# Kernel tuning notes

Hardware: AMD Instinct MI355X
Metric: run time of the kernel (lower is better)

## Reference

```python
import jax, jax.numpy as jnp
import numpy as np

H = 16          # bit depth
N_K = 2         # random masks per flipped bit
TP = 8          # location dims per node
CUR_TP = 4      # dims updated per step
CUR_PORTION = 0.8
N = 1 << H      # location value range
T = 1024        # stations
S = 64          # neighbors per station
D = 256         # embedding dim
C = 2 * H * N_K + 1  # candidate locations per station


def _cos_sim(a, b):
    # frexp-based integer 'cosine' similarity from CritiGraph.cos_similarity
    sg = jnp.where(a >= 0, 1.0, -1.0) * jnp.where(b >= 0, 1.0, -1.0)
    x = ((jnp.abs(a) ^ jnp.abs(b)) + 1).astype(jnp.float32)
    _, e = jnp.frexp(x)  # exponent = bit length of (xor+1)
    return sg * (1.0 - e.astype(jnp.float32) / H)


def _connection(ori, rand_numbers):
    # ori: [T,tp] int64, rand_numbers: [T,H,N_K,tp] int64 in [0, N)
    bits = jnp.int64(1) << jnp.arange(H, dtype=jnp.int64)          # [H]
    flipped = ori[:, None, :] ^ bits[None, :, None]                # [T,H,tp]
    masks = rand_numbers & (bits - 1)[None, :, None, None]        # low-k-bit masks
    res = (flipped[:, :, None, :] ^ masks).reshape(ori.shape[0], H * N_K, TP)
    # candidate order: flipped variants, original (index H*N_K ... wait: res has H*N_K), original, negated
    return jnp.concatenate([res, ori[:, None, :], -res], axis=1)  # [T,C,tp]


def setup_inputs() -> dict:
    key = jax.random.key(0)
    ks = jax.random.split(key, 8)
    return {
        "sta_loc": jax.random.randint(ks[0], (T, TP), 1 - N, N, dtype=jnp.int64),
        "nei_loc": jax.random.randint(ks[1], (T, S, TP), 1 - N, N, dtype=jnp.int64),
        "rand_numbers": jax.random.randint(ks[2], (T, H, N_K, TP), 0, N, dtype=jnp.int64),
        "sta_emb": jax.random.normal(ks[3], (T, D), dtype=jnp.float32),
        "nei_emb": jax.random.normal(ks[4], (T, S, D), dtype=jnp.float32),
        "mask": (jax.random.uniform(ks[5], (T, S)) > 0.1).astype(jnp.float32),
        "rand_vals": jax.random.uniform(ks[6], (T, TP), dtype=jnp.float32),
        "t_rand": jax.random.uniform(ks[7], (T,), dtype=jnp.float32),
    }


def _forward(sta_loc, nei_loc, rand_numbers, sta_emb, nei_emb, mask, rand_vals, t_rand):
    cnc_loc = _connection(sta_loc, rand_numbers)                    # [T,C,tp]
    # euclidean-space cosine targets
    sta_n = sta_emb / jnp.linalg.norm(sta_emb, axis=-1, keepdims=True)
    nei_n = nei_emb / jnp.linalg.norm(nei_emb, axis=-1, keepdims=True)
    eu_val = jnp.einsum("td,tsd->ts", sta_n, nei_n)                 # [T,S]
    # ct_val swap-one-dim kernel (= ct_val_triton math)
    cos_sn = _cos_sim(sta_loc[:, None, :], nei_loc)                 # [T,S,tp]
    cos_sn_sum = cos_sn.sum(axis=-1)                                # [T,S]
    cos_cn = _cos_sim(cnc_loc[:, None, :, :], nei_loc[:, :, None, :])  # [T,S,C,tp]
    ct_val = (cos_sn_sum[:, :, None, None] - cos_sn[:, :, None, :] + cos_cn) / TP
    # masked squared cosine loss (loom_valid)
    lth = mask.sum(axis=1) + 1e-12                                  # [T]
    eu = eu_val[:, :, None, None]
    loss = jnp.square(ct_val - eu) * jnp.abs(eu) * mask[:, :, None, None]
    loss = loss.sum(axis=1) / lth[:, None, None]                    # [T,C,tp]
    # get_best_loc argmin routing
    argmin_all = jnp.argmin(loss, axis=1)                           # [T,tp]
    base = jnp.full((T, TP), H * N_K, dtype=argmin_all.dtype)       # index of original loc
    rand_cols = jnp.argsort(rand_vals, axis=1)[:, :CUR_TP]          # [T,cur_tp]
    sel = t_rand < CUR_PORTION                                      # [T]
    rows = jnp.broadcast_to(jnp.arange(T)[:, None], (T, CUR_TP))
    upd = jnp.where(sel[:, None], argmin_all[rows, rand_cols], base[rows, rand_cols])
    cnc_idx = base.at[rows, rand_cols].set(upd)                     # [T,tp]
    ti = jnp.arange(T)[:, None]
    di = jnp.arange(TP)[None, :]
    selected_locs = cnc_loc[ti, cnc_idx, di]                        # [T,tp]
    real_loss = loss[ti, cnc_idx, di].mean(axis=-1)                 # [T]
    return selected_locs, real_loss


def reference(sta_loc, nei_loc, rand_numbers, sta_emb, nei_emb, mask, rand_vals, t_rand):
    return _forward(sta_loc, nei_loc, rand_numbers, sta_emb, nei_emb, mask, rand_vals, t_rand)
```

## Files before the change

kernel.cpp:

```cpp
#include <hip/hip_runtime.h>
#include <math.h>

#define T_ 1024

__device__ __forceinline__ unsigned icode(int v) {
    return (v < 0) ? (0x80000000u | (unsigned)(-v)) : (unsigned)v;
}

__device__ __forceinline__ float cosc(unsigned ca, unsigned cb) {
    unsigned y = ca ^ cb;
    int x = (int)(y & 0x7fffffffu) + 1;
    float m = fmaf((float)__clz(x), 0.0625f, -1.0f);
    return __uint_as_float(__float_as_uint(m) ^ (y & 0x80000000u));
}

__device__ __forceinline__ int cnc_val(int c, int sl, const int* rn, int p) {
    if (c == 32) return sl;
    int cc = (c < 32) ? c : (c - 33);
    int h = cc >> 1, k = cc & 1;
    int m = rn[h * 16 + k * 8 + p] & ((1 << h) - 1);
    int v = (sl ^ (1 << h)) ^ m;
    return (c < 32) ? v : -v;
}

__global__ __launch_bounds__(256, 4) void critigraph_kernel(
    const int* __restrict__ sta_loc,
    const int* __restrict__ nei_loc,
    const int* __restrict__ rand_numbers,
    const float* __restrict__ sta_emb,
    const float* __restrict__ nei_emb,
    const float* __restrict__ mask,
    const float* __restrict__ rand_vals,
    const float* __restrict__ t_rand,
    float* __restrict__ out_sel,
    float* __restrict__ out_loss)
{
    const int t = blockIdx.x;
    const int tid = threadIdx.x;
    const int srow = tid >> 2, j4 = tid & 3;
    const int c = tid >> 3, p = tid & 7;

    __shared__ __align__(16) float    s_sta[256];
    __shared__ __align__(16) unsigned s_nlc[512];
    __shared__ __align__(16) int      s_rn[256];
    __shared__ __align__(8)  float2   s_cg[512];
    __shared__ __align__(8)  float2   s_ew[64];
    __shared__ float  s_css[64];
    __shared__ float  s_loss[520];
    __shared__ int    s_sl[8];
    __shared__ unsigned s_slc[8];
    __shared__ float  s_m[64];
    __shared__ float  s_rv[8];
    __shared__ float  s_lth;

    float stav = sta_emb[t * 256 + tid];
    int nl0 = nei_loc[t * 512 + tid];
    int nl1 = nei_loc[t * 512 + 256 + tid];
    int rnv = rand_numbers[t * 256 + tid];
    int slv = 0; float rvv = 0.f;
    if (tid < 8) { slv = sta_loc[t * 8 + tid]; rvv = rand_vals[t * 8 + tid]; }
    float mv = (tid < 64) ? mask[t * 64 + tid] : 0.f;
    float trv = t_rand[t];

    const float4* nrow = reinterpret_cast<const float4*>(nei_emb + (size_t)t * 64 * 256);
    float4 nv[16];
#pragma unroll
    for (int i = 0; i < 16; i++) nv[i] = nrow[srow * 64 + i * 4 + j4];

    s_sta[tid] = stav;
    s_nlc[tid]       = icode(nl0);
    s_nlc[tid + 256] = icode(nl1);
    s_rn[tid] = rnv;
    if (tid < 8) { s_sl[tid] = slv; s_slc[tid] = icode(slv); s_rv[tid] = rvv; }
    if (tid < 64) s_m[tid] = mv;
    __syncthreads();

    if ((tid >> 6) == 1) {
        float x = s_m[tid & 63];
#pragma unroll
        for (int off = 32; off; off >>= 1) x += __shfl_xor(x, off, 64);
        if ((tid & 63) == 0) s_lth = x + 1e-12f;
    }

    {
        unsigned slc[8];
#pragma unroll
        for (int i = 0; i < 8; i++) slc[i] = s_slc[i];
        const uint4* nl4 = reinterpret_cast<const uint4*>(s_nlc);
        const int s0 = tid >> 3;
#pragma unroll
        for (int half = 0; half < 2; half++) {
            int s = s0 + half * 32;
            uint4 ra = nl4[s * 2], rb = nl4[s * 2 + 1];
            unsigned nn[8] = {ra.x, ra.y, ra.z, ra.w, rb.x, rb.y, rb.z, rb.w};
            float css = 0.f, csm[8];
#pragma unroll
            for (int i = 0; i < 8; i++) { csm[i] = cosc(slc[i], nn[i]); css += csm[i]; }
            if (p == 0) s_css[s] = css;
            s_cg[s * 8 + p] = make_float2(__uint_as_float(nn[p]), css - csm[p]);
        }
    }

    {
        const float4* st4 = reinterpret_cast<const float4*>(s_sta);
        float d0 = 0.f, n0 = 0.f, a0 = 0.f;
#pragma unroll
        for (int i = 0; i < 16; i++) {
            float4 sv = st4[i * 4 + j4];
            float4 nn = nv[i];
            d0 = fmaf(nn.x, sv.x, d0); d0 = fmaf(nn.y, sv.y, d0);
            d0 = fmaf(nn.z, sv.z, d0); d0 = fmaf(nn.w, sv.w, d0);
            n0 = fmaf(nn.x, nn.x, n0); n0 = fmaf(nn.y, nn.y, n0);
            n0 = fmaf(nn.z, nn.z, n0); n0 = fmaf(nn.w, nn.w, n0);
            a0 = fmaf(sv.x, sv.x, a0); a0 = fmaf(sv.y, sv.y, a0);
            a0 = fmaf(sv.z, sv.z, a0); a0 = fmaf(sv.w, sv.w, a0);
        }
        d0 += __shfl_xor(d0, 1, 64); d0 += __shfl_xor(d0, 2, 64);
        n0 += __shfl_xor(n0, 1, 64); n0 += __shfl_xor(n0, 2, 64);
        a0 += __shfl_xor(a0, 1, 64); a0 += __shfl_xor(a0, 2, 64);
        if (j4 == 0) {
            float eun = d0 * (1.0f / sqrtf(n0));
            float eu  = eun * (1.0f / sqrtf(a0));
            float w   = fabsf(eu) * s_m[srow];
            s_ew[srow] = make_float2(eu, w);
        }
    }

    int vcn = cnc_val(c, s_sl[p], s_rn, p);
    unsigned avc  = icode(vcn);
    unsigned flip = (vcn != 0) ? 0x80000000u : 0u;
    __syncthreads();

    {
        float acc1 = 0.f, acc2 = 0.f;
#pragma unroll 4
        for (int s = 0; s < 64; s++) {
            float2 cg = s_cg[s * 8 + p];
            float2 ew = s_ew[s];
            unsigned y = avc ^ __float_as_uint(cg.x);
            int x = (int)(y & 0x7fffffffu) + 1;
            float m1 = fmaf((float)__clz(x), 0.0625f, -1.0f);
            unsigned cb = __float_as_uint(m1) ^ (y & 0x80000000u);
            float cc1 = __uint_as_float(cb);
            float cc2 = __uint_as_float(cb ^ flip);
            float d1 = fmaf(cg.y + cc1, 0.125f, -ew.x);
            float d2 = fmaf(cg.y + cc2, 0.125f, -ew.x);
            acc1 = fmaf(d1 * d1, ew.y, acc1);
            acc2 = fmaf(d2 * d2, ew.y, acc2);
        }
        float lth = s_lth;
        s_loss[c * 8 + p]        = acc1 / lth;
        s_loss[(c + 33) * 8 + p] = acc2 / lth;
        if (tid < 8) {
            float a32 = 0.f;
            for (int s = 0; s < 64; s++) {
                float2 ew = s_ew[s];
                float d = fmaf(s_css[s], 0.125f, -ew.x);
                a32 = fmaf(d * d, ew.y, a32);
            }
            s_loss[256 + tid] = a32 / lth;
        }
    }
    __syncthreads();

    if (tid < 64) {
        const int pp = tid >> 3, g = tid & 7;
        float bv = s_loss[g * 8 + pp];
        int bi = g;
#pragma unroll
        for (int k = 1; k < 8; k++) {
            float vv = s_loss[(g + 8 * k) * 8 + pp];
            if (vv < bv) { bv = vv; bi = g + 8 * k; }
        }
        if (g == 0) {
            float vv = s_loss[512 + pp];
            if (vv < bv) { bv = vv; bi = 64; }
        }
#pragma unroll
        for (int off = 1; off < 8; off <<= 1) {
            float ov = __shfl_xor(bv, off, 64);
            int   oi = __shfl_xor(bi, off, 64);
            if (ov < bv || (ov == bv && oi < bi)) { bv = ov; bi = oi; }
        }
        bool sel = trv < 0.8f;
        float rme = s_rv[pp];
        int rank = 0;
#pragma unroll
        for (int p2 = 0; p2 < 8; p2++) {
            float ro = s_rv[p2];
            rank += (ro < rme || (ro == rme && p2 < pp)) ? 1 : 0;
        }
        int cidx = (rank < 4 && sel) ? bi : 32;
        if (g == 0)
            out_sel[t * 8 + pp] = (float)cnc_val(cidx, s_sl[pp], s_rn, pp);
        float a = 0.f;
#pragma unroll
        for (int p2 = 0; p2 < 8; p2++) {
            int cx = __shfl(cidx, p2 * 8, 64);
            a += s_loss[cx * 8 + p2];
        }
        if (tid == 0) out_loss[t] = a * 0.125f;
    }
}

extern "C" void kernel_launch(void* const* d_in, const int* in_sizes, int n_in,
                              void* d_out, int out_size, void* d_ws, size_t ws_size,
                              hipStream_t stream) {
    const int*   sta_loc      = (const int*)d_in[0];
    const int*   nei_loc      = (const int*)d_in[1];
    const int*   rand_numbers = (const int*)d_in[2];
    const float* sta_emb      = (const float*)d_in[3];
    const float* nei_emb      = (const float*)d_in[4];
    const float* mask         = (const float*)d_in[5];
    const float* rand_vals    = (const float*)d_in[6];
    const float* t_rand       = (const float*)d_in[7];

    float* out_sel  = (float*)d_out;
    float* out_loss = out_sel + T_ * 8;

    critigraph_kernel<<<T_, 256, 0, stream>>>(
        sta_loc, nei_loc, rand_numbers, sta_emb, nei_emb, mask,
        rand_vals, t_rand, out_sel, out_loss);
}
```

Baseline: 113.0 us.

## Double block size so each thread handles one candidate and half a row

```diff
diff --git a/kernel.cpp b/kernel.cpp
--- a/kernel.cpp
+++ b/kernel.cpp
@@ -23,7 +23,7 @@
     return (c < 32) ? v : -v;
 }
 
-__global__ __launch_bounds__(256, 4) void critigraph_kernel(
+__global__ __launch_bounds__(512, 4) void critigraph_kernel(
     const int* __restrict__ sta_loc,
     const int* __restrict__ nei_loc,
     const int* __restrict__ rand_numbers,
@@ -37,7 +37,7 @@
 {
     const int t = blockIdx.x;
     const int tid = threadIdx.x;
-    const int srow = tid >> 2, j4 = tid & 3;
+    const int srow = tid >> 3, j8 = tid & 7;
     const int c = tid >> 3, p = tid & 7;
 
     __shared__ __align__(16) float    s_sta[256];
@@ -45,7 +45,6 @@
     __shared__ __align__(16) int      s_rn[256];
     __shared__ __align__(8)  float2   s_cg[512];
     __shared__ __align__(8)  float2   s_ew[64];
-    __shared__ float  s_css[64];
     __shared__ float  s_loss[520];
     __shared__ int    s_sl[8];
     __shared__ unsigned s_slc[8];
@@ -53,24 +52,21 @@
     __shared__ float  s_rv[8];
     __shared__ float  s_lth;
 
-    float stav = sta_emb[t * 256 + tid];
-    int nl0 = nei_loc[t * 512 + tid];
-    int nl1 = nei_loc[t * 512 + 256 + tid];
-    int rnv = rand_numbers[t * 256 + tid];
+    float stav = (tid < 256) ? sta_emb[t * 256 + tid] : 0.f;
+    int   nlv  = nei_loc[t * 512 + tid];
+    int   rnv  = (tid < 256) ? rand_numbers[t * 256 + tid] : 0;
     int slv = 0; float rvv = 0.f;
     if (tid < 8) { slv = sta_loc[t * 8 + tid]; rvv = rand_vals[t * 8 + tid]; }
     float mv = (tid < 64) ? mask[t * 64 + tid] : 0.f;
     float trv = t_rand[t];
 
     const float4* nrow = reinterpret_cast<const float4*>(nei_emb + (size_t)t * 64 * 256);
-    float4 nv[16];
-#pragma unroll
-    for (int i = 0; i < 16; i++) nv[i] = nrow[srow * 64 + i * 4 + j4];
-
-    s_sta[tid] = stav;
-    s_nlc[tid]       = icode(nl0);
-    s_nlc[tid + 256] = icode(nl1);
-    s_rn[tid] = rnv;
+    float4 nv[8];
+#pragma unroll
+    for (int i = 0; i < 8; i++) nv[i] = nrow[srow * 64 + i * 8 + j8];
+
+    if (tid < 256) { s_sta[tid] = stav; s_rn[tid] = rnv; }
+    s_nlc[tid] = icode(nlv);
     if (tid < 8) { s_sl[tid] = slv; s_slc[tid] = icode(slv); s_rv[tid] = rvv; }
     if (tid < 64) s_m[tid] = mv;
     __syncthreads();
@@ -83,30 +79,21 @@
     }
 
     {
-        unsigned slc[8];
-#pragma unroll
-        for (int i = 0; i < 8; i++) slc[i] = s_slc[i];
         const uint4* nl4 = reinterpret_cast<const uint4*>(s_nlc);
-        const int s0 = tid >> 3;
-#pragma unroll
-        for (int half = 0; half < 2; half++) {
-            int s = s0 + half * 32;
-            uint4 ra = nl4[s * 2], rb = nl4[s * 2 + 1];
-            unsigned nn[8] = {ra.x, ra.y, ra.z, ra.w, rb.x, rb.y, rb.z, rb.w};
-            float css = 0.f, csm[8];
-#pragma unroll
-            for (int i = 0; i < 8; i++) { csm[i] = cosc(slc[i], nn[i]); css += csm[i]; }
-            if (p == 0) s_css[s] = css;
-            s_cg[s * 8 + p] = make_float2(__uint_as_float(nn[p]), css - csm[p]);
-        }
+        uint4 ra = nl4[srow * 2], rb = nl4[srow * 2 + 1];
+        unsigned nn[8] = {ra.x, ra.y, ra.z, ra.w, rb.x, rb.y, rb.z, rb.w};
+        float css = 0.f, csm[8];
+#pragma unroll
+        for (int i = 0; i < 8; i++) { csm[i] = cosc(s_slc[i], nn[i]); css += csm[i]; }
+        s_cg[srow * 8 + j8] = make_float2(__uint_as_float(nn[j8]), css - csm[j8]);
     }
 
     {
         const float4* st4 = reinterpret_cast<const float4*>(s_sta);
         float d0 = 0.f, n0 = 0.f, a0 = 0.f;
 #pragma unroll
-        for (int i = 0; i < 16; i++) {
-            float4 sv = st4[i * 4 + j4];
+        for (int i = 0; i < 8; i++) {
+            float4 sv = st4[i * 8 + j8];
             float4 nn = nv[i];
             d0 = fmaf(nn.x, sv.x, d0); d0 = fmaf(nn.y, sv.y, d0);
             d0 = fmaf(nn.z, sv.z, d0); d0 = fmaf(nn.w, sv.w, d0);
@@ -115,10 +102,10 @@
             a0 = fmaf(sv.x, sv.x, a0); a0 = fmaf(sv.y, sv.y, a0);
             a0 = fmaf(sv.z, sv.z, a0); a0 = fmaf(sv.w, sv.w, a0);
         }
-        d0 += __shfl_xor(d0, 1, 64); d0 += __shfl_xor(d0, 2, 64);
-        n0 += __shfl_xor(n0, 1, 64); n0 += __shfl_xor(n0, 2, 64);
-        a0 += __shfl_xor(a0, 1, 64); a0 += __shfl_xor(a0, 2, 64);
-        if (j4 == 0) {
+        d0 += __shfl_xor(d0, 1, 64); d0 += __shfl_xor(d0, 2, 64); d0 += __shfl_xor(d0, 4, 64);
+        n0 += __shfl_xor(n0, 1, 64); n0 += __shfl_xor(n0, 2, 64); n0 += __shfl_xor(n0, 4, 64);
+        a0 += __shfl_xor(a0, 1, 64); a0 += __shfl_xor(a0, 2, 64); a0 += __shfl_xor(a0, 4, 64);
+        if (j8 == 0) {
             float eun = d0 * (1.0f / sqrtf(n0));
             float eu  = eun * (1.0f / sqrtf(a0));
             float w   = fabsf(eu) * s_m[srow];
@@ -126,13 +113,13 @@
         }
     }
 
-    int vcn = cnc_val(c, s_sl[p], s_rn, p);
-    unsigned avc  = icode(vcn);
-    unsigned flip = (vcn != 0) ? 0x80000000u : 0u;
+    unsigned avc = icode(cnc_val(c, s_sl[p], s_rn, p));
+    unsigned avc64 = 0;
+    if (tid < 8) avc64 = icode(cnc_val(64, s_sl[tid], s_rn, tid));
     __syncthreads();
 
     {
-        float acc1 = 0.f, acc2 = 0.f;
+        float acc = 0.f;
 #pragma unroll 4
         for (int s = 0; s < 64; s++) {
             float2 cg = s_cg[s * 8 + p];
@@ -140,25 +127,25 @@
             unsigned y = avc ^ __float_as_uint(cg.x);
             int x = (int)(y & 0x7fffffffu) + 1;
             float m1 = fmaf((float)__clz(x), 0.0625f, -1.0f);
-            unsigned cb = __float_as_uint(m1) ^ (y & 0x80000000u);
-            float cc1 = __uint_as_float(cb);
-            float cc2 = __uint_as_float(cb ^ flip);
-            float d1 = fmaf(cg.y + cc1, 0.125f, -ew.x);
-            float d2 = fmaf(cg.y + cc2, 0.125f, -ew.x);
-            acc1 = fmaf(d1 * d1, ew.y, acc1);
-            acc2 = fmaf(d2 * d2, ew.y, acc2);
+            float cc = __uint_as_float(__float_as_uint(m1) ^ (y & 0x80000000u));
+            float d = fmaf(cg.y + cc, 0.125f, -ew.x);
+            acc = fmaf(d * d, ew.y, acc);
         }
         float lth = s_lth;
-        s_loss[c * 8 + p]        = acc1 / lth;
-        s_loss[(c + 33) * 8 + p] = acc2 / lth;
+        s_loss[c * 8 + p] = acc / lth;
         if (tid < 8) {
-            float a32 = 0.f;
+            float a64 = 0.f;
             for (int s = 0; s < 64; s++) {
+                float2 cg = s_cg[s * 8 + tid];
                 float2 ew = s_ew[s];
-                float d = fmaf(s_css[s], 0.125f, -ew.x);
-                a32 = fmaf(d * d, ew.y, a32);
+                unsigned y = avc64 ^ __float_as_uint(cg.x);
+                int x = (int)(y & 0x7fffffffu) + 1;
+                float m1 = fmaf((float)__clz(x), 0.0625f, -1.0f);
+                float cc = __uint_as_float(__float_as_uint(m1) ^ (y & 0x80000000u));
+                float d = fmaf(cg.y + cc, 0.125f, -ew.x);
+                a64 = fmaf(d * d, ew.y, a64);
             }
-            s_loss[256 + tid] = a32 / lth;
+            s_loss[512 + tid] = a64 / lth;
         }
     }
     __syncthreads();
@@ -218,7 +205,7 @@
     float* out_sel  = (float*)d_out;
     float* out_loss = out_sel + T_ * 8;
 
-    critigraph_kernel<<<T_, 256, 0, stream>>>(
+    critigraph_kernel<<<T_, 512, 0, stream>>>(
         sta_loc, nei_loc, rand_numbers, sta_emb, nei_emb, mask,
         rand_vals, t_rand, out_sel, out_loss);
 }
```

After: 114.5 us. Within noise of the previous version (+1.3%).
